# Performance work log

Hardware: AMD Instinct MI355X
Metric: run time of the kernel (lower is better)

Reference implementation:

```python
import jax, jax.numpy as jnp
import numpy as np

E = 16          # expert_num
T = 8192        # token_num
H = 1024        # hidden_size
I = 4096        # intermediate_size
LN_EPS = 1e-12


def setup_inputs() -> dict:
    key = jax.random.key(0)
    ks = jax.random.split(key, 6)
    hidden_states = jax.random.normal(ks[0], (T, H), dtype=jnp.float32)
    perm = jax.random.permutation(ks[1], T).astype(jnp.int32)
    s1 = 1.0 / np.sqrt(H)
    s2 = 1.0 / np.sqrt(I)
    w1 = jax.random.uniform(ks[2], (E, I, H), jnp.float32, -s1, s1)
    b1 = jax.random.uniform(ks[3], (E, I), jnp.float32, -s1, s1)
    w2 = jax.random.uniform(ks[4], (E, H, I), jnp.float32, -s2, s2)
    b2 = jax.random.uniform(ks[5], (E, H), jnp.float32, -s2, s2)
    ln_gamma = jnp.ones((H,), jnp.float32)
    ln_beta = jnp.zeros((H,), jnp.float32)
    return {"hidden_states": hidden_states, "perm": perm, "w1": w1, "b1": b1,
            "w2": w2, "b2": b2, "ln_gamma": ln_gamma, "ln_beta": ln_beta}


def _layer_norm(x, gamma, beta, eps):
    mu = jnp.mean(x, axis=-1, keepdims=True)
    var = jnp.var(x, axis=-1, keepdims=True)
    return (x - mu) * jax.lax.rsqrt(var + eps) * gamma + beta


def reference(hidden_states, perm, w1, b1, w2, b2, ln_gamma, ln_beta):
    # dispatch: gather tokens by random permutation, group per expert
    xp = hidden_states[perm].reshape(E, T // E, H)            # [E, T/E, H]
    # grouped expert FFN (batched GEMM replaces the per-expert Python loop)
    h = jnp.einsum('eth,eih->eti', xp, w1) + b1[:, None, :]   # [E, T/E, I]
    h = jax.nn.gelu(h, approximate=False)
    o = jnp.einsum('eti,ehi->eth', h, w2) + b2[:, None, :]    # [E, T/E, H]
    # scatter-restore via inverse permutation
    restore = jnp.argsort(perm)
    o = o.reshape(T, H)[restore]
    # dropout is identity (p=0, eval); residual + LayerNorm
    return _layer_norm(o + hidden_states, ln_gamma, ln_beta, LN_EPS)
```

## Files before the change

### kernel.cpp

```cpp
#include <hip/hip_runtime.h>
#include <hip/hip_bf16.h>
#include <stdint.h>

#define E_NUM 16
#define T_NUM 8192
#define H_DIM 1024
#define I_DIM 4096
#define MPE   512

typedef __attribute__((ext_vector_type(8))) short short8;
typedef __attribute__((ext_vector_type(4))) float f32x4;
using bf16 = __hip_bfloat16;

typedef const __attribute__((address_space(1))) void GLV;
typedef __attribute__((address_space(3))) void LDSV;

__device__ __forceinline__ uint32_t pack2_bf16(float a, float b) {
  union { float f; uint32_t u; } ua, ub;
  ua.f = a; ub.f = b;
  uint32_t x = ua.u + (0x7FFFu + ((ua.u >> 16) & 1u));
  uint32_t y = ub.u + (0x7FFFu + ((ub.u >> 16) & 1u));
  return (x >> 16) | (y & 0xFFFF0000u);
}

__device__ __forceinline__ uint2 cvt4u(float4 a) {
  union { uint2 u; __hip_bfloat162 h[2]; } r;
  r.h[0] = __float22bfloat162_rn({a.x, a.y});
  r.h[1] = __float22bfloat162_rn({a.z, a.w});
  return r.u;
}

__device__ __forceinline__ float fast_gelu(float x) {
  const float p = x * fmaf(x * x, -0.0713548162726f, -1.59576912161f);
  return x * __builtin_amdgcn_rcpf(1.0f + __expf(p));
}

__global__ __launch_bounds__(256)
void gather_cast_kernel(const float* __restrict__ hs, const int* __restrict__ perm,
                        uint32_t* __restrict__ xp) {
  const int r = blockIdx.x;
  const int t = threadIdx.x;
  const int src = perm[r];
  float4 v = ((const float4*)(hs + (size_t)src * H_DIM))[t];
  uint2 o;
  o.x = pack2_bf16(v.x, v.y);
  o.y = pack2_bf16(v.z, v.w);
  ((uint2*)(xp + (size_t)r * (H_DIM / 2)))[t] = o;
}

template<int EPI, int KSPLIT, int N, int KFULL, int KLEN, int LOG_NBN>
__global__ __launch_bounds__(1024, 4)
void moe_gemm_kernel(const bf16* __restrict__ A, const float* __restrict__ Bw,
                     const float* __restrict__ bias, bf16* __restrict__ Hout,
                     float* __restrict__ Pout) {
  constexpr int NK = KLEN / 32;
  __shared__ bf16 As[3][512 * 32];
  __shared__ bf16 Bs[3][64 * 64];

  const int nwg = gridDim.x, qx = nwg >> 3, orig = blockIdx.x;
  const int wg = (orig & 7) * qx + (orig >> 3);
  const int bn   = wg & ((1 << LOG_NBN) - 1);
  const int rest = wg >> LOG_NBN;
  const int ks = (KSPLIT == 2) ? (rest & 1) : 0;
  const int e  = (KSPLIT == 2) ? (rest >> 1) : rest;
  const int K0 = ks * KLEN;

  const int tid = threadIdx.x;
  const int l = tid & 63;
  const int w = tid >> 6;
  const int wr = w >> 1, wc = w & 1;
  const int fr = l & 15, fq = l >> 4;
  const int rx = fr & 7;

  const bf16*  Ae = A  + (size_t)e * MPE * KFULL + K0;
  const float* Be = Bw + ((size_t)e * N + (size_t)bn * 128) * KFULL + K0;

  const int apq = tid >> 3;
  const int ag  = (tid & 7) ^ (apq & 7);
  const bf16* As0 = Ae + (size_t)(apq       + 256 * (ag >> 2)) * KFULL + (ag & 3) * 8;
  const bf16* As1 = Ae + (size_t)(apq + 128 + 256 * (ag >> 2)) * KFULL + (ag & 3) * 8;

  const int bc = tid >> 3, bsg = tid & 7;
  const float* Bsrc = Be + (size_t)bc * KFULL + bsg * 4;
  const int bp  = bc & 63;
  const int bwo = bp * 64 + (((((bc >> 6) << 2) | (bsg >> 1)) ^ (bp & 7)) << 3)
                + (bsg & 1) * 4;

  const int aso = (((((wr >> 2) << 2)) | fq) ^ rx) * 8;
  const int bro = fr * 64 + ((((wc << 2) | fq) ^ rx) << 3);

  f32x4 acc[4][4];
#pragma unroll
  for (int m = 0; m < 4; ++m)
#pragma unroll
    for (int n = 0; n < 4; ++n) acc[m][n] = (f32x4){0.f, 0.f, 0.f, 0.f};

  float4 s0, s1;

#define ISSUE_A(buf, kt)                                                            \
  {                                                                                 \
    __builtin_amdgcn_global_load_lds((GLV*)(As0 + (kt) * 32),                       \
                                     (LDSV*)&As[buf][tid * 8], 16, 0, 0);           \
    __builtin_amdgcn_global_load_lds((GLV*)(As1 + (kt) * 32),                       \
                                     (LDSV*)&As[buf][(1024 + tid) * 8], 16, 0, 0);  \
  }
#define ISSUE_B(dst, kt)  { dst = *(const float4*)(Bsrc + (kt) * 32); }
#define WRITE_B(buf, src) { *(uint2*)&Bs[buf][bwo] = cvt4u(src); }

  ISSUE_A(0, 0); ISSUE_B(s0, 0);
  ISSUE_A(1, 1); ISSUE_B(s1, 1);
  asm volatile("s_waitcnt vmcnt(3)" ::: "memory");
  __builtin_amdgcn_sched_barrier(0);
  WRITE_B(0, s0);
  asm volatile("s_waitcnt lgkmcnt(0)" ::: "memory");
  __builtin_amdgcn_sched_barrier(0);
  __builtin_amdgcn_s_barrier();
  __builtin_amdgcn_sched_barrier(0);

  int bufc = 0, bufn1 = 1, bufn2 = 2;
  for (int t = 0; t < NK; ++t) {
    if (t + 2 < NK) {
      ISSUE_A(bufn2, t + 2);
      if ((t & 1) == 0) { ISSUE_B(s0, t + 2); } else { ISSUE_B(s1, t + 2); }
      asm volatile("s_waitcnt vmcnt(3)" ::: "memory");
      __builtin_amdgcn_sched_barrier(0);
    } else {
      asm volatile("s_waitcnt vmcnt(0)" ::: "memory");
      __builtin_amdgcn_sched_barrier(0);
    }
    if (t + 1 < NK) {
      if ((t & 1) == 0) { WRITE_B(bufn1, s1); } else { WRITE_B(bufn1, s0); }
    }

    short8 a8[4];
#pragma unroll
    for (int m = 0; m < 4; ++m)
      a8[m] = *(const short8*)&As[bufc][((wr & 3) * 64 + m * 16 + fr) * 64 + aso];
    short8 b8[4];
#pragma unroll
    for (int n = 0; n < 4; ++n)
      b8[n] = *(const short8*)&Bs[bufc][bro + n * 1024];
#pragma unroll
    for (int m = 0; m < 4; ++m)
#pragma unroll
      for (int n = 0; n < 4; ++n)
        acc[m][n] = __builtin_amdgcn_mfma_f32_16x16x32_bf16(a8[m], b8[n], acc[m][n], 0, 0, 0);

    asm volatile("s_waitcnt lgkmcnt(0)" ::: "memory");
    __builtin_amdgcn_sched_barrier(0);
    __builtin_amdgcn_s_barrier();
    __builtin_amdgcn_sched_barrier(0);

    const int b0 = bufc;
    bufc = bufn1; bufn1 = bufn2; bufn2 = b0;
  }
#undef ISSUE_A
#undef ISSUE_B
#undef WRITE_B
  __syncthreads();

  if (EPI == 1) {
    float bv[4];
#pragma unroll
    for (int n = 0; n < 4; ++n)
      bv[n] = bias[(size_t)e * N + bn * 128 + wc * 64 + n * 16 + fr];
    bf16* He = Hout + (size_t)e * MPE * N;

    bf16* Ls = &As[0][0];
#pragma unroll
    for (int P = 0; P < 2; ++P) {
      if ((wr >> 2) == P) {
        const int wrl = wr & 3;
#pragma unroll
        for (int m = 0; m < 4; ++m) {
#pragma unroll
          for (int j = 0; j < 4; ++j) {
            const int lr = wrl * 64 + m * 16 + fq * 4 + j;
#pragma unroll
            for (int n = 0; n < 4; ++n) {
              const int c = wc * 64 + n * 16 + fr;
              const int byteoff = lr * 256 + ((c * 2) ^ ((lr & 7) << 4));
              Ls[byteoff >> 1] = __float2bfloat16(fast_gelu(acc[m][n][j] + bv[n]));
            }
          }
        }
      }
      __syncthreads();
#pragma unroll
      for (int q = 0; q < 4; ++q) {
        const int o = (tid + q * 1024) * 16;
        const int lr = o >> 8;
        const int cb = o & 255;
        const int sb = lr * 256 + (cb ^ ((lr & 7) << 4));
        uint4 v = *(const uint4*)((const char*)Ls + sb);
        *(uint4*)&He[(size_t)(P * 256 + lr) * N + bn * 128 + (cb >> 1)] = v;
      }
      __syncthreads();
    }
  } else {
    float* Pd = Pout + (size_t)ks * T_NUM * H_DIM + (size_t)e * MPE * N;
#pragma unroll
    for (int m = 0; m < 4; ++m) {
#pragma unroll
      for (int j = 0; j < 4; ++j) {
        const int row = wr * 64 + m * 16 + fq * 4 + j;
#pragma unroll
        for (int n = 0; n < 4; ++n) {
          const int col = bn * 128 + wc * 64 + n * 16 + fr;
          Pd[(size_t)row * N + col] = acc[m][n][j];
        }
      }
    }
  }
}

__global__ __launch_bounds__(256)
void ln_resid2_kernel(float* __restrict__ out, const float* __restrict__ hs,
                      const float* __restrict__ p0, const float* __restrict__ p1,
                      const float* __restrict__ b2, const float* __restrict__ gamma,
                      const float* __restrict__ beta, const int* __restrict__ perm,
                      const int two) {
  const int r = blockIdx.x;
  const int t = threadIdx.x;
  const int e = r >> 9;
  const int drow = perm[r];
  float4 a = ((const float4*)(p0 + (size_t)r * H_DIM))[t];
  if (two) {
    float4 b = ((const float4*)(p1 + (size_t)r * H_DIM))[t];
    a.x += b.x; a.y += b.y; a.z += b.z; a.w += b.w;
  }
  float4 bb = ((const float4*)(b2 + (size_t)e * H_DIM))[t];
  float4 h  = ((const float4*)(hs + (size_t)drow * H_DIM))[t];
  float v0 = a.x + bb.x + h.x, v1 = a.y + bb.y + h.y;
  float v2 = a.z + bb.z + h.z, v3 = a.w + bb.w + h.w;
  float s  = v0 + v1 + v2 + v3;
  float sq = v0 * v0 + v1 * v1 + v2 * v2 + v3 * v3;
#pragma unroll
  for (int off = 32; off > 0; off >>= 1) {
    s  += __shfl_down(s, off);
    sq += __shfl_down(sq, off);
  }
  __shared__ float ss[4], ssq[4];
  const int wv = t >> 6;
  if ((t & 63) == 0) { ss[wv] = s; ssq[wv] = sq; }
  __syncthreads();
  s  = ss[0] + ss[1] + ss[2] + ss[3];
  sq = ssq[0] + ssq[1] + ssq[2] + ssq[3];
  const float mu  = s * (1.0f / (float)H_DIM);
  const float var = sq * (1.0f / (float)H_DIM) - mu * mu;
  const float rs  = rsqrtf(var + 1e-12f);
  float4 g = ((const float4*)gamma)[t];
  float4 b = ((const float4*)beta)[t];
  float4 rr;
  rr.x = (v0 - mu) * rs * g.x + b.x;
  rr.y = (v1 - mu) * rs * g.y + b.y;
  rr.z = (v2 - mu) * rs * g.z + b.z;
  rr.w = (v3 - mu) * rs * g.w + b.w;
  ((float4*)(out + (size_t)drow * H_DIM))[t] = rr;
}

extern "C" void kernel_launch(void* const* d_in, const int* in_sizes, int n_in,
                              void* d_out, int out_size, void* d_ws, size_t ws_size,
                              hipStream_t stream) {
  const float* hs    = (const float*)d_in[0];
  const int*   perm  = (const int*)d_in[1];
  const float* w1    = (const float*)d_in[2];
  const float* b1    = (const float*)d_in[3];
  const float* w2    = (const float*)d_in[4];
  const float* b2    = (const float*)d_in[5];
  const float* gamma = (const float*)d_in[6];
  const float* beta  = (const float*)d_in[7];
  float* out = (float*)d_out;

  const size_t xp_b   = (size_t)T_NUM * H_DIM * sizeof(bf16);
  const size_t hbuf_b = (size_t)T_NUM * I_DIM * sizeof(bf16);
  const size_t part_b = (size_t)T_NUM * H_DIM * sizeof(float);

  bf16*  xp   = (bf16*)d_ws;
  bf16*  hbuf = (bf16*)((char*)d_ws + xp_b);
  float* pbuf = (float*)((char*)d_ws + xp_b + hbuf_b);

  gather_cast_kernel<<<T_NUM, 256, 0, stream>>>(hs, perm, (uint32_t*)xp);

  moe_gemm_kernel<1, 1, I_DIM, H_DIM, H_DIM, 5>
      <<<512, 1024, 0, stream>>>(xp, w1, b1, hbuf, nullptr);

  if (ws_size >= xp_b + hbuf_b + 2 * part_b) {
    moe_gemm_kernel<0, 2, H_DIM, I_DIM, I_DIM / 2, 3>
        <<<256, 1024, 0, stream>>>(hbuf, w2, nullptr, nullptr, pbuf);
    ln_resid2_kernel<<<T_NUM, 256, 0, stream>>>(out, hs, pbuf, pbuf + (size_t)T_NUM * H_DIM,
                                                b2, gamma, beta, perm, 1);
  } else {
    moe_gemm_kernel<0, 1, H_DIM, I_DIM, I_DIM, 3>
        <<<128, 1024, 0, stream>>>(hbuf, w2, nullptr, nullptr, pbuf);
    ln_resid2_kernel<<<T_NUM, 256, 0, stream>>>(out, hs, pbuf, nullptr,
                                                b2, gamma, beta, perm, 0);
  }
}
```

Baseline: 320.6 us.

## Switch GEMM main loop from triple to double buffering

```diff
diff --git a/kernel.cpp b/kernel.cpp
--- a/kernel.cpp
+++ b/kernel.cpp
@@ -54,8 +54,8 @@
                      const float* __restrict__ bias, bf16* __restrict__ Hout,
                      float* __restrict__ Pout) {
   constexpr int NK = KLEN / 32;
-  __shared__ bf16 As[3][512 * 32];
-  __shared__ bf16 Bs[3][64 * 64];
+  __shared__ bf16 As[2][512 * 32];
+  __shared__ bf16 Bs[2][64 * 64];
 
   const int nwg = gridDim.x, qx = nwg >> 3, orig = blockIdx.x;
   const int wg = (orig & 7) * qx + (orig >> 3);
@@ -95,67 +95,58 @@
 #pragma unroll
     for (int n = 0; n < 4; ++n) acc[m][n] = (f32x4){0.f, 0.f, 0.f, 0.f};
 
-  float4 s0, s1;
-
-#define ISSUE_A(buf, kt)                                                            \
+  float4 breg;
+
+#define ISSUE(buf, kt)                                                              \
   {                                                                                 \
+    breg = *(const float4*)(Bsrc + (kt) * 32);                                      \
     __builtin_amdgcn_global_load_lds((GLV*)(As0 + (kt) * 32),                       \
                                      (LDSV*)&As[buf][tid * 8], 16, 0, 0);           \
     __builtin_amdgcn_global_load_lds((GLV*)(As1 + (kt) * 32),                       \
                                      (LDSV*)&As[buf][(1024 + tid) * 8], 16, 0, 0);  \
   }
-#define ISSUE_B(dst, kt)  { dst = *(const float4*)(Bsrc + (kt) * 32); }
-#define WRITE_B(buf, src) { *(uint2*)&Bs[buf][bwo] = cvt4u(src); }
-
-  ISSUE_A(0, 0); ISSUE_B(s0, 0);
-  ISSUE_A(1, 1); ISSUE_B(s1, 1);
-  asm volatile("s_waitcnt vmcnt(3)" ::: "memory");
+#define WRITE_B(buf) { *(uint2*)&Bs[buf][bwo] = cvt4u(breg); }
+
+  ISSUE(0, 0);
+  asm volatile("s_waitcnt vmcnt(2)" ::: "memory");
   __builtin_amdgcn_sched_barrier(0);
-  WRITE_B(0, s0);
-  asm volatile("s_waitcnt lgkmcnt(0)" ::: "memory");
+  WRITE_B(0);
+  asm volatile("s_waitcnt vmcnt(0) lgkmcnt(0)" ::: "memory");
   __builtin_amdgcn_sched_barrier(0);
   __builtin_amdgcn_s_barrier();
   __builtin_amdgcn_sched_barrier(0);
 
-  int bufc = 0, bufn1 = 1, bufn2 = 2;
   for (int t = 0; t < NK; ++t) {
-    if (t + 2 < NK) {
-      ISSUE_A(bufn2, t + 2);
-      if ((t & 1) == 0) { ISSUE_B(s0, t + 2); } else { ISSUE_B(s1, t + 2); }
-      asm volatile("s_waitcnt vmcnt(3)" ::: "memory");
+    const int cur = t & 1, nxt = cur ^ 1;
+    const bool more = (t + 1) < NK;
+
+    if (more) ISSUE(nxt, t + 1);
+
+    short8 a8[4];
+#pragma unroll
+    for (int m = 0; m < 4; ++m)
+      a8[m] = *(const short8*)&As[cur][((wr & 3) * 64 + m * 16 + fr) * 64 + aso];
+    short8 b8[4];
+#pragma unroll
+    for (int n = 0; n < 4; ++n)
+      b8[n] = *(const short8*)&Bs[cur][bro + n * 1024];
+#pragma unroll
+    for (int m = 0; m < 4; ++m)
+#pragma unroll
+      for (int n = 0; n < 4; ++n)
+        acc[m][n] = __builtin_amdgcn_mfma_f32_16x16x32_bf16(a8[m], b8[n], acc[m][n], 0, 0, 0);
+
+    if (more) {
+      asm volatile("s_waitcnt vmcnt(2)" ::: "memory");
       __builtin_amdgcn_sched_barrier(0);
-    } else {
-      asm volatile("s_waitcnt vmcnt(0)" ::: "memory");
+      WRITE_B(nxt);
+      asm volatile("s_waitcnt vmcnt(0) lgkmcnt(0)" ::: "memory");
+      __builtin_amdgcn_sched_barrier(0);
+      __builtin_amdgcn_s_barrier();
       __builtin_amdgcn_sched_barrier(0);
     }
-    if (t + 1 < NK) {
-      if ((t & 1) == 0) { WRITE_B(bufn1, s1); } else { WRITE_B(bufn1, s0); }
-    }
-
-    short8 a8[4];
-#pragma unroll
-    for (int m = 0; m < 4; ++m)
-      a8[m] = *(const short8*)&As[bufc][((wr & 3) * 64 + m * 16 + fr) * 64 + aso];
-    short8 b8[4];
-#pragma unroll
-    for (int n = 0; n < 4; ++n)
-      b8[n] = *(const short8*)&Bs[bufc][bro + n * 1024];
-#pragma unroll
-    for (int m = 0; m < 4; ++m)
-#pragma unroll
-      for (int n = 0; n < 4; ++n)
-        acc[m][n] = __builtin_amdgcn_mfma_f32_16x16x32_bf16(a8[m], b8[n], acc[m][n], 0, 0, 0);
-
-    asm volatile("s_waitcnt lgkmcnt(0)" ::: "memory");
-    __builtin_amdgcn_sched_barrier(0);
-    __builtin_amdgcn_s_barrier();
-    __builtin_amdgcn_sched_barrier(0);
-
-    const int b0 = bufc;
-    bufc = bufn1; bufn1 = bufn2; bufn2 = b0;
-  }
-#undef ISSUE_A
-#undef ISSUE_B
+  }
+#undef ISSUE
 #undef WRITE_B
   __syncthreads();
 
```

Measured after the change: 293.8 us. -8.4%, faster.
